# Kernel tuning notes

Measured on AMD Instinct MI355X. Metric: run time of the kernel, lower is better.

## Reference

```python
import jax, jax.numpy as jnp
import numpy as np

L, T, E, D, H, B = 2, 8, 2, 128, 128, 32768
NE = T * E  # total experts per layer = 16


def setup_inputs() -> dict:
    key = jax.random.key(0)
    ks = jax.random.split(key, 8)
    s = 1.0 / np.sqrt(D)
    inputs = jax.random.normal(ks[0], (B, T, D), dtype=jnp.float32)
    w1 = jax.random.uniform(ks[1], (L, NE, D, H), jnp.float32, -s, s)
    b1 = jax.random.uniform(ks[2], (L, NE, H), jnp.float32, -s, s)
    w2 = jax.random.uniform(ks[3], (L, NE, H, H), jnp.float32, -s, s)
    b2 = jax.random.uniform(ks[4], (L, NE, H), jnp.float32, -s, s)
    gate_w = jax.random.uniform(ks[5], (L, T, D, NE), jnp.float32, -s, s)
    gate_b = jax.random.uniform(ks[6], (L, T, NE), jnp.float32, -s, s)
    se = 1.0 / np.sqrt(E)
    sew = jax.random.uniform(ks[7], (L, T, E), jnp.float32, -se, se)
    return {"inputs": inputs, "w1": w1, "b1": b1, "w2": w2, "b2": b2,
            "gate_w": gate_w, "gate_b": gate_b, "sew": sew}


def reference(inputs, w1, b1, w2, b2, gate_w, gate_b, sew):
    x = inputs  # [B, T, D]
    for l in range(L):
        # each task's input feeds its num_task_experts experts
        x_exp = jnp.repeat(x, E, axis=1)  # [B, NE, D]
        h = jax.nn.relu(jnp.einsum('bed,edh->beh', x_exp, w1[l]) + b1[l])
        eo = jax.nn.relu(jnp.einsum('beh,eho->beo', h, w2[l]) + b2[l])  # [B, NE, H]
        # per-task gating over all experts
        gates = jax.nn.softmax(jnp.einsum('btd,tde->bte', x, gate_w[l]) + gate_b[l], axis=-1)  # [B, T, NE]
        fused = jnp.einsum('bte,beh->bth', gates, eo)  # [B, T, H]
        # self-expert residual (num_task_experts > 1 branch)
        eo_r = eo.reshape(eo.shape[0], T, E, -1)  # [B, T, E, H]
        fused = fused + jnp.einsum('te,bteh->bth', sew[l], eo_r)
        x = fused
    return x
```

## Files before the change

kernel.cpp:

```cpp
#include <hip/hip_runtime.h>


typedef float f32x4 __attribute__((ext_vector_type(4)));
typedef _Float16 f16;
typedef f16 f16x8 __attribute__((ext_vector_type(8)));
typedef f16 f16x4 __attribute__((ext_vector_type(4)));

#define MFMA(a, b, c) __builtin_amdgcn_mfma_f32_16x16x32_f16(a, b, c, 0, 0, 0)
#define LOSC (1.0f / 2048.0f)
#define AS1 __attribute__((address_space(1)))
#define AS3 __attribute__((address_space(3)))

__device__ __forceinline__ void split2h(float f, f16& h, f16& l) {
  h = (f16)f;
  l = (f16)((f - (float)h) * 2048.0f);
}

__global__ __launch_bounds__(256) void kprep(
    const float* __restrict__ x0, const float* __restrict__ w1,
    const float* __restrict__ w2, const float* __restrict__ gw,
    f16* __restrict__ x0h, f16* __restrict__ w1T, f16* __restrict__ w2T,
    f16* __restrict__ gwT) {
  int bid = blockIdx.x;
  int tid = threadIdx.x;
  if (bid < 16384) {
    size_t i = ((size_t)bid * 256 + tid) * 8;
    f32x4 f0 = *(const f32x4*)(x0 + i);
    f32x4 f1 = *(const f32x4*)(x0 + i + 4);
    f16x8 v;
#pragma unroll
    for (int z = 0; z < 4; ++z) {
      v[z] = (f16)f0[z];
      v[4 + z] = (f16)f1[z];
    }
    *(f16x8*)(x0h + i) = v;
    return;
  }
  int idx = (bid - 16384) * 256 + tid;
  if (idx < 131072) {
    const float* src = (idx < 65536) ? w1 : w2;
    f16* dst = (idx < 65536) ? w1T : w2T;
    int i = idx & 65535;
    int lane = i & 63;
    int it = (i >> 6) & 7;
    int ks = (i >> 9) & 3;
    int q = i >> 11;
    int g = lane >> 4, le = lane & 15;
    f16x8 vh;
#pragma unroll
    for (int j = 0; j < 8; ++j)
      vh[j] = (f16)src[((size_t)q * 128 + (32 * ks + 8 * g + j)) * 128 + 16 * it + le];
    *(f16x8*)(dst + (size_t)i * 8) = vh;
  } else {
    int i = idx - 131072;
    int lane = i & 63;
    int ks = (i >> 6) & 3;
    int q = (i >> 8) & 15;
    int g = lane >> 4, le = lane & 15;
    f16x8 vh, vl;
#pragma unroll
    for (int j = 0; j < 8; ++j) {
      float f = gw[((size_t)q * 128 + (32 * ks + 8 * g + j)) * 16 + le];
      f16 h, l;
      split2h(f, h, l);
      vh[j] = h;
      vl[j] = l;
    }
    *(f16x8*)(gwT + (size_t)i * 8) = vh;
    *(f16x8*)(gwT + 32768 + (size_t)i * 8) = vl;
  }
}

__global__ __launch_bounds__(256, 2) void kexp(
    const f16* __restrict__ xs, const f16* __restrict__ w1T,
    const f16* __restrict__ w2T, const float* __restrict__ b1,
    const float* __restrict__ b2, f16* __restrict__ eo, int layer) {
  __shared__ f16 sX[2][8192];
  __shared__ f16 sH[8192];
  __shared__ f16 sEO[8192];
  const int tid = threadIdx.x;
  const int lane = tid & 63;
  const int wave = tid >> 6;
  const int jh = wave & 1, oh = wave >> 1;
  const int g = lane >> 4, le = lane & 15;
  const int e = blockIdx.x & 15;
  const int r0 = (blockIdx.x >> 4) * 1024;
  const int te = e >> 1;
  const int lx = layer * 16 + e;

  f16x8 w1r[4][4], w2r[4][4];
#pragma unroll
  for (int it = 0; it < 4; ++it)
#pragma unroll
    for (int ks = 0; ks < 4; ++ks) {
      size_t fb = ((size_t)((lx * 4 + ks) * 8 + 4 * oh + it) * 64 + lane) * 8;
      w1r[it][ks] = *(const f16x8*)(w1T + fb);
      w2r[it][ks] = *(const f16x8*)(w2T + fb);
    }
  f32x4 b1v[4], b2v[4];
#pragma unroll
  for (int it = 0; it < 4; ++it) {
    b1v[it] = *(const f32x4*)(b1 + lx * 128 + 64 * oh + 16 * it + 4 * g);
    b2v[it] = *(const f32x4*)(b2 + lx * 128 + 64 * oh + 16 * it + 4 * g);
  }

  auto stage_gl = [&](int buf, int tile) {
#pragma unroll
    for (int i = 0; i < 4; ++i) {
      int row = 16 * wave + 4 * i + (lane >> 4);
      int gc = lane & 15;
      const f16* src = xs + ((size_t)(r0 + tile * 64 + row) * 8 + te) * 128 +
                       (gc ^ (row & 7)) * 8;
      f16* dst = &sX[buf][(16 * wave + 4 * i) * 128];
      __builtin_amdgcn_global_load_lds((const AS1 void*)src, (AS3 void*)dst,
                                       16, 0, 0);
    }
  };
  auto eo_flush = [&](int tile) {
#pragma unroll
    for (int i = 0; i < 4; ++i) {
      int slot = i * 256 + tid;
      int row = slot >> 4, c = slot & 15;
      f16x8 v = *(const f16x8*)(&sEO[row * 128 + 8 * (c ^ (row & 7))]);
      *(f16x8*)(eo + ((size_t)e * 32768 + (r0 + tile * 64 + row)) * 128 + 8 * c) = v;
    }
  };

  stage_gl(0, 0);
  __syncthreads();

  for (int tile = 0; tile < 16; ++tile) {
    const int b = tile & 1;
    if (tile < 15) stage_gl(b ^ 1, tile + 1);
    if (tile > 0) eo_flush(tile - 1);
    {
      f32x4 a[4][2];
#pragma unroll
      for (int it = 0; it < 4; ++it)
#pragma unroll
        for (int j2 = 0; j2 < 2; ++j2) a[it][j2] = f32x4{0.f, 0.f, 0.f, 0.f};
#pragma unroll
      for (int ks = 0; ks < 4; ++ks)
#pragma unroll
        for (int j2 = 0; j2 < 2; ++j2) {
          int brow = 32 * jh + 16 * j2 + le;
          f16x8 bf = *(const f16x8*)(&sX[b][brow * 128 + 8 * ((4 * ks + g) ^ (brow & 7))]);
#pragma unroll
          for (int it = 0; it < 4; ++it)
            a[it][j2] = MFMA(w1r[it][ks], bf, a[it][j2]);
        }
#pragma unroll
      for (int it = 0; it < 4; ++it)
#pragma unroll
        for (int j2 = 0; j2 < 2; ++j2) {
          int brow = 32 * jh + 16 * j2 + le;
          f16x4 hv;
#pragma unroll
          for (int r = 0; r < 4; ++r)
            hv[r] = (f16)fmaxf(a[it][j2][r] + b1v[it][r], 0.f);
          int gran = 8 * oh + 2 * it + (g >> 1);
          *(f16x4*)(&sH[brow * 128 + 8 * (gran ^ (brow & 7)) + 4 * (g & 1)]) = hv;
        }
    }
    __syncthreads();
    {
      f32x4 a[4][2];
#pragma unroll
      for (int it = 0; it < 4; ++it)
#pragma unroll
        for (int j2 = 0; j2 < 2; ++j2) a[it][j2] = f32x4{0.f, 0.f, 0.f, 0.f};
#pragma unroll
      for (int ks = 0; ks < 4; ++ks)
#pragma unroll
        for (int j2 = 0; j2 < 2; ++j2) {
          int brow = 32 * jh + 16 * j2 + le;
          f16x8 bf = *(const f16x8*)(&sH[brow * 128 + 8 * ((4 * ks + g) ^ (brow & 7))]);
#pragma unroll
          for (int it = 0; it < 4; ++it)
            a[it][j2] = MFMA(w2r[it][ks], bf, a[it][j2]);
        }
#pragma unroll
      for (int it = 0; it < 4; ++it)
#pragma unroll
        for (int j2 = 0; j2 < 2; ++j2) {
          int brow = 32 * jh + 16 * j2 + le;
          f16x4 ev;
#pragma unroll
          for (int r = 0; r < 4; ++r)
            ev[r] = (f16)fmaxf(a[it][j2][r] + b2v[it][r], 0.f);
          int gran = 8 * oh + 2 * it + (g >> 1);
          *(f16x4*)(&sEO[brow * 128 + 8 * (gran ^ (brow & 7)) + 4 * (g & 1)]) = ev;
        }
    }
#pragma unroll
    for (int it = 0; it < 4; ++it)
#pragma unroll
      for (int ks = 0; ks < 4; ++ks) {
        asm volatile("" : "+v"(w1r[it][ks]));
        asm volatile("" : "+v"(w2r[it][ks]));
      }
    __syncthreads();
  }
  eo_flush(15);
}

__global__ __launch_bounds__(512, 4) void kmix(
    const f16* __restrict__ xs, const f16* __restrict__ gwT,
    const float* __restrict__ gb, const float* __restrict__ sw,
    const f16* __restrict__ eo, f16* __restrict__ x1out,
    float* __restrict__ fout, int layer) {
  __shared__ float sG[8 * 16 * 32];
  const int tid = threadIdx.x;
  const int lane = tid & 63;
  const int t = tid >> 6;
  const int g = lane >> 4, le = lane & 15;
  const int r0 = blockIdx.x * 32;
  const int lt = layer * 8 + t;

  {
    f32x4 l1[2], l2[2];
#pragma unroll
    for (int j = 0; j < 2; ++j) {
      l1[j] = f32x4{0.f, 0.f, 0.f, 0.f};
      l2[j] = f32x4{0.f, 0.f, 0.f, 0.f};
    }
#pragma unroll
    for (int ks = 0; ks < 4; ++ks) {
      size_t fb = ((size_t)(lt * 4 + ks) * 64 + lane) * 8;
      f16x8 ah = *(const f16x8*)(gwT + fb);
      f16x8 al = *(const f16x8*)(gwT + 32768 + fb);
#pragma unroll
      for (int j = 0; j < 2; ++j) {
        f16x8 bf = *(const f16x8*)(xs + ((size_t)(r0 + 16 * j + le) * 8 + t) * 128 +
                                   32 * ks + 8 * g);
        l1[j] = MFMA(ah, bf, l1[j]);
        l2[j] = MFMA(al, bf, l2[j]);
      }
    }
#pragma unroll
    for (int j = 0; j < 2; ++j) {
      float zb[4];
#pragma unroll
      for (int r = 0; r < 4; ++r)
        zb[r] = l1[j][r] + l2[j][r] * LOSC + gb[lt * 16 + 4 * g + r];
      float m4 = fmaxf(fmaxf(zb[0], zb[1]), fmaxf(zb[2], zb[3]));
      m4 = fmaxf(m4, __shfl_xor(m4, 16, 64));
      m4 = fmaxf(m4, __shfl_xor(m4, 32, 64));
      float p4[4], s4 = 0.f;
#pragma unroll
      for (int r = 0; r < 4; ++r) {
        p4[r] = __expf(zb[r] - m4);
        s4 += p4[r];
      }
      s4 += __shfl_xor(s4, 16, 64);
      s4 += __shfl_xor(s4, 32, 64);
      float inv = 1.f / s4;
#pragma unroll
      for (int r = 0; r < 4; ++r)
        sG[(t * 16 + 4 * g + r) * 32 + 16 * j + le] = p4[r] * inv;
    }
  }
  __syncthreads();

  const int lrow = tid >> 4;
  const int grow = r0 + lrow;
  const int cq = (tid & 15) * 8;
  f32x4 am[8][2];
#pragma unroll
  for (int tt = 0; tt < 8; ++tt)
#pragma unroll
    for (int k = 0; k < 2; ++k) am[tt][k] = f32x4{0.f, 0.f, 0.f, 0.f};

  for (int ee = 0; ee < 16; ++ee) {
    const int tte = ee >> 1, eh = ee & 1;
    f16x8 ev = *(const f16x8*)(eo + ((size_t)ee * 32768 + grow) * 128 + cq);
    float evf[8];
#pragma unroll
    for (int z = 0; z < 8; ++z) evf[z] = (float)ev[z];
    float ssew = sw[(layer * 8 + tte) * 2 + eh];
#pragma unroll
    for (int tt = 0; tt < 8; ++tt) {
      float coef = sG[(tt * 16 + ee) * 32 + lrow] + (tt == tte ? ssew : 0.f);
#pragma unroll
      for (int z = 0; z < 8; ++z)
        am[tt][z >> 2][z & 3] = fmaf(coef, evf[z], am[tt][z >> 2][z & 3]);
    }
  }
#pragma unroll
  for (int tt = 0; tt < 8; ++tt) {
    size_t off = ((size_t)grow * 8 + tt) * 128 + cq;
    if (layer == 0) {
      f16x8 hv;
#pragma unroll
      for (int z = 0; z < 8; ++z) hv[z] = (f16)am[tt][z >> 2][z & 3];
      *(f16x8*)(x1out + off) = hv;
    } else {
      *(f32x4*)(fout + off) = am[tt][0];
      *(f32x4*)(fout + off + 4) = am[tt][1];
    }
  }
}

extern "C" void kernel_launch(void* const* d_in, const int* in_sizes, int n_in,
                              void* d_out, int out_size, void* d_ws, size_t ws_size,
                              hipStream_t stream) {
  const float* x0 = (const float*)d_in[0];
  const float* w1 = (const float*)d_in[1];
  const float* b1 = (const float*)d_in[2];
  const float* w2 = (const float*)d_in[3];
  const float* b2 = (const float*)d_in[4];
  const float* gw = (const float*)d_in[5];
  const float* gb = (const float*)d_in[6];
  const float* sw = (const float*)d_in[7];

  f16* w1T = (f16*)d_ws;
  f16* w2T = (f16*)((char*)d_ws + 1048576);
  f16* gwT = (f16*)((char*)d_ws + 2097152);
  f16* x0h = (f16*)((char*)d_ws + 4194304);
  f16* x1h = (f16*)((char*)d_ws + 71303168);
  f16* eo = (f16*)((char*)d_ws + 138412032);
  float* out = (float*)d_out;

  kprep<<<16912, 256, 0, stream>>>(x0, w1, w2, gw, x0h, w1T, w2T, gwT);

  kexp<<<512, 256, 0, stream>>>(x0h, w1T, w2T, b1, b2, eo, 0);
  kmix<<<1024, 512, 0, stream>>>(x0h, gwT, gb, sw, eo, x1h, nullptr, 0);
  kexp<<<512, 256, 0, stream>>>(x1h, w1T, w2T, b1, b2, eo, 1);
  kmix<<<1024, 512, 0, stream>>>(x1h, gwT, gb, sw, eo, nullptr, out, 1);
}
```

Measured before the change: 269.7 us.

## Software-pipeline expert GEMMs with double-buffered hidden tile and direct EO stores

Restructures the expert kernel loop so GEMM1 of tile i and GEMM2 of tile i-1 run in the same iteration, with the hidden activation double-buffered in LDS. This halves the block barriers per tile. The EO LDS staging buffer and flush are dropped, and results are written straight from registers as 8-byte stores, trading coalescing for less LDS traffic. It also remaps block indices so consecutive blocks are spread across XCDs, and moves the register-pinning asm barriers out of the loop, which could let the compiler spill or reload weights.

```diff
diff --git a/kernel.cpp b/kernel.cpp
--- a/kernel.cpp
+++ b/kernel.cpp
@@ -76,15 +76,15 @@
     const f16* __restrict__ w2T, const float* __restrict__ b1,
     const float* __restrict__ b2, f16* __restrict__ eo, int layer) {
   __shared__ f16 sX[2][8192];
-  __shared__ f16 sH[8192];
-  __shared__ f16 sEO[8192];
+  __shared__ f16 sH[2][8192];
   const int tid = threadIdx.x;
   const int lane = tid & 63;
   const int wave = tid >> 6;
   const int jh = wave & 1, oh = wave >> 1;
   const int g = lane >> 4, le = lane & 15;
-  const int e = blockIdx.x & 15;
-  const int r0 = (blockIdx.x >> 4) * 1024;
+  const int wg = (blockIdx.x & 7) * 64 + (blockIdx.x >> 3);
+  const int e = wg & 15;
+  const int r0 = (wg >> 4) * 1024;
   const int te = e >> 1;
   const int lx = layer * 16 + e;
 
@@ -116,92 +116,86 @@
                                        16, 0, 0);
     }
   };
-  auto eo_flush = [&](int tile) {
-#pragma unroll
-    for (int i = 0; i < 4; ++i) {
-      int slot = i * 256 + tid;
-      int row = slot >> 4, c = slot & 15;
-      f16x8 v = *(const f16x8*)(&sEO[row * 128 + 8 * (c ^ (row & 7))]);
-      *(f16x8*)(eo + ((size_t)e * 32768 + (r0 + tile * 64 + row)) * 128 + 8 * c) = v;
-    }
+
+  auto gemm1 = [&](int b) {
+    f32x4 a[4][2];
+#pragma unroll
+    for (int it = 0; it < 4; ++it)
+#pragma unroll
+      for (int j2 = 0; j2 < 2; ++j2) a[it][j2] = f32x4{0.f, 0.f, 0.f, 0.f};
+#pragma unroll
+    for (int ks = 0; ks < 4; ++ks)
+#pragma unroll
+      for (int j2 = 0; j2 < 2; ++j2) {
+        int brow = 32 * jh + 16 * j2 + le;
+        f16x8 bf = *(const f16x8*)(&sX[b][brow * 128 + 8 * ((4 * ks + g) ^ (brow & 7))]);
+#pragma unroll
+        for (int it = 0; it < 4; ++it)
+          a[it][j2] = MFMA(w1r[it][ks], bf, a[it][j2]);
+      }
+#pragma unroll
+    for (int it = 0; it < 4; ++it)
+#pragma unroll
+      for (int j2 = 0; j2 < 2; ++j2) {
+        int brow = 32 * jh + 16 * j2 + le;
+        f16x4 hv;
+#pragma unroll
+        for (int r = 0; r < 4; ++r)
+          hv[r] = (f16)fmaxf(a[it][j2][r] + b1v[it][r], 0.f);
+        int gran = 8 * oh + 2 * it + (g >> 1);
+        *(f16x4*)(&sH[b][brow * 128 + 8 * (gran ^ (brow & 7)) + 4 * (g & 1)]) = hv;
+      }
+  };
+
+  auto gemm2 = [&](int tile, int hb) {
+    f32x4 a[4][2];
+#pragma unroll
+    for (int it = 0; it < 4; ++it)
+#pragma unroll
+      for (int j2 = 0; j2 < 2; ++j2) a[it][j2] = f32x4{0.f, 0.f, 0.f, 0.f};
+#pragma unroll
+    for (int ks = 0; ks < 4; ++ks)
+#pragma unroll
+      for (int j2 = 0; j2 < 2; ++j2) {
+        int brow = 32 * jh + 16 * j2 + le;
+        f16x8 bf = *(const f16x8*)(&sH[hb][brow * 128 + 8 * ((4 * ks + g) ^ (brow & 7))]);
+#pragma unroll
+        for (int it = 0; it < 4; ++it)
+          a[it][j2] = MFMA(w2r[it][ks], bf, a[it][j2]);
+      }
+#pragma unroll
+    for (int it = 0; it < 4; ++it)
+#pragma unroll
+      for (int j2 = 0; j2 < 2; ++j2) {
+        int grow = r0 + tile * 64 + 32 * jh + 16 * j2 + le;
+        f16x4 ev;
+#pragma unroll
+        for (int r = 0; r < 4; ++r)
+          ev[r] = (f16)fmaxf(a[it][j2][r] + b2v[it][r], 0.f);
+        *(f16x4*)(eo + ((size_t)e * 32768 + grow) * 128 + 64 * oh + 16 * it +
+                  4 * g) = ev;
+      }
   };
 
   stage_gl(0, 0);
   __syncthreads();
 
-  for (int tile = 0; tile < 16; ++tile) {
-    const int b = tile & 1;
-    if (tile < 15) stage_gl(b ^ 1, tile + 1);
-    if (tile > 0) eo_flush(tile - 1);
-    {
-      f32x4 a[4][2];
-#pragma unroll
-      for (int it = 0; it < 4; ++it)
-#pragma unroll
-        for (int j2 = 0; j2 < 2; ++j2) a[it][j2] = f32x4{0.f, 0.f, 0.f, 0.f};
-#pragma unroll
-      for (int ks = 0; ks < 4; ++ks)
-#pragma unroll
-        for (int j2 = 0; j2 < 2; ++j2) {
-          int brow = 32 * jh + 16 * j2 + le;
-          f16x8 bf = *(const f16x8*)(&sX[b][brow * 128 + 8 * ((4 * ks + g) ^ (brow & 7))]);
-#pragma unroll
-          for (int it = 0; it < 4; ++it)
-            a[it][j2] = MFMA(w1r[it][ks], bf, a[it][j2]);
-        }
-#pragma unroll
-      for (int it = 0; it < 4; ++it)
-#pragma unroll
-        for (int j2 = 0; j2 < 2; ++j2) {
-          int brow = 32 * jh + 16 * j2 + le;
-          f16x4 hv;
-#pragma unroll
-          for (int r = 0; r < 4; ++r)
-            hv[r] = (f16)fmaxf(a[it][j2][r] + b1v[it][r], 0.f);
-          int gran = 8 * oh + 2 * it + (g >> 1);
-          *(f16x4*)(&sH[brow * 128 + 8 * (gran ^ (brow & 7)) + 4 * (g & 1)]) = hv;
-        }
-    }
+  for (int i = 0; i < 16; ++i) {
+    const int b = i & 1;
+    if (i < 15) stage_gl(b ^ 1, i + 1);
+    gemm1(b);
+    if (i > 0) gemm2(i - 1, b ^ 1);
     __syncthreads();
-    {
-      f32x4 a[4][2];
-#pragma unroll
-      for (int it = 0; it < 4; ++it)
-#pragma unroll
-        for (int j2 = 0; j2 < 2; ++j2) a[it][j2] = f32x4{0.f, 0.f, 0.f, 0.f};
-#pragma unroll
-      for (int ks = 0; ks < 4; ++ks)
-#pragma unroll
-        for (int j2 = 0; j2 < 2; ++j2) {
-          int brow = 32 * jh + 16 * j2 + le;
-          f16x8 bf = *(const f16x8*)(&sH[brow * 128 + 8 * ((4 * ks + g) ^ (brow & 7))]);
-#pragma unroll
-          for (int it = 0; it < 4; ++it)
-            a[it][j2] = MFMA(w2r[it][ks], bf, a[it][j2]);
-        }
-#pragma unroll
-      for (int it = 0; it < 4; ++it)
-#pragma unroll
-        for (int j2 = 0; j2 < 2; ++j2) {
-          int brow = 32 * jh + 16 * j2 + le;
-          f16x4 ev;
-#pragma unroll
-          for (int r = 0; r < 4; ++r)
-            ev[r] = (f16)fmaxf(a[it][j2][r] + b2v[it][r], 0.f);
-          int gran = 8 * oh + 2 * it + (g >> 1);
-          *(f16x4*)(&sEO[brow * 128 + 8 * (gran ^ (brow & 7)) + 4 * (g & 1)]) = ev;
-        }
-    }
-#pragma unroll
-    for (int it = 0; it < 4; ++it)
-#pragma unroll
-      for (int ks = 0; ks < 4; ++ks) {
-        asm volatile("" : "+v"(w1r[it][ks]));
-        asm volatile("" : "+v"(w2r[it][ks]));
-      }
-    __syncthreads();
-  }
-  eo_flush(15);
+  }
+  gemm2(15, 1);
+
+#pragma unroll
+  for (int it = 0; it < 4; ++it)
+#pragma unroll
+    for (int ks = 0; ks < 4; ++ks) {
+      asm volatile("" : "+v"(w1r[it][ks]));
+      asm volatile("" : "+v"(w2r[it][ks]));
+    }
 }
 
 __global__ __launch_bounds__(512, 4) void kmix(
```

After: 291.2 us. 8.0% more time.

## Compute layer-0 gating softmax in fp32 inside prep kernel

Applied to the files above, without the earlier changes.

The prep kernel now stages the input rows in shared memory and computes the layer-0 gate logits and softmax in full fp32 while it converts x to fp16. The gates are written to a workspace buffer that kmix reads for layer 0 instead of running its split-fp16 MFMA gate GEMM. This moves gate work off the mixing kernel and uses exact fp32 inputs. The cost is a scalar 128-long dot product per thread in prep, extra global traffic for the gate buffer, and a larger prep block size.

```diff
diff --git a/kernel.cpp b/kernel.cpp
--- a/kernel.cpp
+++ b/kernel.cpp
@@ -16,27 +16,51 @@
   l = (f16)((f - (float)h) * 2048.0f);
 }
 
-__global__ __launch_bounds__(256) void kprep(
+__global__ __launch_bounds__(1024) void kprep(
     const float* __restrict__ x0, const float* __restrict__ w1,
     const float* __restrict__ w2, const float* __restrict__ gw,
-    f16* __restrict__ x0h, f16* __restrict__ w1T, f16* __restrict__ w2T,
-    f16* __restrict__ gwT) {
-  int bid = blockIdx.x;
-  int tid = threadIdx.x;
-  if (bid < 16384) {
-    size_t i = ((size_t)bid * 256 + tid) * 8;
-    f32x4 f0 = *(const f32x4*)(x0 + i);
-    f32x4 f1 = *(const f32x4*)(x0 + i + 4);
+    const float* __restrict__ gb, f16* __restrict__ x0h,
+    f16* __restrict__ w1T, f16* __restrict__ w2T, f16* __restrict__ gwT,
+    float* __restrict__ g0) {
+  const int bid = blockIdx.x;
+  const int tid = threadIdx.x;
+  if (bid < 4096) {
+    __shared__ float xs[8192];
+    size_t base = (size_t)bid * 8192 + tid * 8;
+    f32x4 f0 = *(const f32x4*)(x0 + base);
+    f32x4 f1 = *(const f32x4*)(x0 + base + 4);
     f16x8 v;
 #pragma unroll
     for (int z = 0; z < 4; ++z) {
       v[z] = (f16)f0[z];
       v[4 + z] = (f16)f1[z];
     }
-    *(f16x8*)(x0h + i) = v;
+    *(f16x8*)(x0h + base) = v;
+    *(f32x4*)(&xs[tid * 8]) = f0;
+    *(f32x4*)(&xs[tid * 8 + 4]) = f1;
+    __syncthreads();
+    const int r8 = tid >> 7, t = (tid >> 4) & 7, e = tid & 15;
+    const float* gwp = gw + (size_t)t * 2048 + e;
+    const float* xr = &xs[r8 * 1024 + t * 128];
+    float acc = 0.f;
+#pragma unroll 8
+    for (int d = 0; d < 128; ++d) acc = fmaf(xr[d], gwp[d * 16], acc);
+    acc += gb[t * 16 + e];
+    float m = acc;
+    m = fmaxf(m, __shfl_xor(m, 1, 64));
+    m = fmaxf(m, __shfl_xor(m, 2, 64));
+    m = fmaxf(m, __shfl_xor(m, 4, 64));
+    m = fmaxf(m, __shfl_xor(m, 8, 64));
+    float p = __expf(acc - m);
+    float s = p;
+    s += __shfl_xor(s, 1, 64);
+    s += __shfl_xor(s, 2, 64);
+    s += __shfl_xor(s, 4, 64);
+    s += __shfl_xor(s, 8, 64);
+    g0[((size_t)(bid * 8 + r8) * 8 + t) * 16 + e] = p / s;
     return;
   }
-  int idx = (bid - 16384) * 256 + tid;
+  int idx = (bid - 4096) * 1024 + tid;
   if (idx < 131072) {
     const float* src = (idx < 65536) ? w1 : w2;
     f16* dst = (idx < 65536) ? w1T : w2T;
@@ -207,9 +231,9 @@
 __global__ __launch_bounds__(512, 4) void kmix(
     const f16* __restrict__ xs, const f16* __restrict__ gwT,
     const float* __restrict__ gb, const float* __restrict__ sw,
-    const f16* __restrict__ eo, f16* __restrict__ x1out,
-    float* __restrict__ fout, int layer) {
-  __shared__ float sG[8 * 16 * 32];
+    const float* __restrict__ g0, const f16* __restrict__ eo,
+    f16* __restrict__ x1out, float* __restrict__ fout, int layer) {
+  __shared__ float sB[4096];
   const int tid = threadIdx.x;
   const int lane = tid & 63;
   const int t = tid >> 6;
@@ -217,7 +241,11 @@
   const int r0 = blockIdx.x * 32;
   const int lt = layer * 8 + t;
 
-  {
+  if (layer == 0) {
+    *(f32x4*)(&sB[tid * 8]) = *(const f32x4*)(g0 + (size_t)r0 * 128 + tid * 8);
+    *(f32x4*)(&sB[tid * 8 + 4]) =
+        *(const f32x4*)(g0 + (size_t)r0 * 128 + tid * 8 + 4);
+  } else {
     f32x4 l1[2], l2[2];
 #pragma unroll
     for (int j = 0; j < 2; ++j) {
@@ -257,7 +285,7 @@
       float inv = 1.f / s4;
 #pragma unroll
       for (int r = 0; r < 4; ++r)
-        sG[(t * 16 + 4 * g + r) * 32 + 16 * j + le] = p4[r] * inv;
+        sB[(t * 16 + 4 * g + r) * 32 + 16 * j + le] = p4[r] * inv;
     }
   }
   __syncthreads();
@@ -280,7 +308,9 @@
     float ssew = sw[(layer * 8 + tte) * 2 + eh];
 #pragma unroll
     for (int tt = 0; tt < 8; ++tt) {
-      float coef = sG[(tt * 16 + ee) * 32 + lrow] + (tt == tte ? ssew : 0.f);
+      float coef = ((layer == 0) ? sB[lrow * 128 + tt * 16 + ee]
+                                 : sB[(tt * 16 + ee) * 32 + lrow]) +
+                   (tt == tte ? ssew : 0.f);
 #pragma unroll
       for (int z = 0; z < 8; ++z)
         am[tt][z >> 2][z & 3] = fmaf(coef, evf[z], am[tt][z >> 2][z & 3]);
@@ -319,12 +349,13 @@
   f16* x0h = (f16*)((char*)d_ws + 4194304);
   f16* x1h = (f16*)((char*)d_ws + 71303168);
   f16* eo = (f16*)((char*)d_ws + 138412032);
+  float* g0 = (float*)((char*)d_ws + 272629760);
   float* out = (float*)d_out;
 
-  kprep<<<16912, 256, 0, stream>>>(x0, w1, w2, gw, x0h, w1T, w2T, gwT);
+  kprep<<<4228, 1024, 0, stream>>>(x0, w1, w2, gw, gb, x0h, w1T, w2T, gwT, g0);
 
   kexp<<<512, 256, 0, stream>>>(x0h, w1T, w2T, b1, b2, eo, 0);
-  kmix<<<1024, 512, 0, stream>>>(x0h, gwT, gb, sw, eo, x1h, nullptr, 0);
+  kmix<<<1024, 512, 0, stream>>>(x0h, gwT, gb, sw, g0, eo, x1h, nullptr, 0);
   kexp<<<512, 256, 0, stream>>>(x1h, w1T, w2T, b1, b2, eo, 1);
-  kmix<<<1024, 512, 0, stream>>>(x1h, gwT, gb, sw, eo, nullptr, out, 1);
-}
+  kmix<<<1024, 512, 0, stream>>>(x1h, gwT, gb, sw, g0, eo, nullptr, out, 1);
+}
```

Result: slower. 313.4 us (+16.2%).
